# Kernel tuning notes

Measured on AMD Instinct MI355X. Metric: run time of the kernel, lower is better.

## Reference

```python
import jax, jax.numpy as jnp
import numpy as np

IN_FEATURES = 4096
OUT_FEATURES = 16384
BATCH, SEQ = 4, 2048


def setup_inputs() -> dict:
    key = jax.random.key(0)
    k_x, k_w, k_b = jax.random.split(key, 3)
    x = jax.random.normal(k_x, (BATCH, SEQ, IN_FEATURES), dtype=jnp.float32)
    # int8-valued quantized weight stored as int32 for portability (values in [-128, 127])
    weight_quantized = jax.random.randint(k_w, (OUT_FEATURES, IN_FEATURES), -128, 128, dtype=jnp.int32)
    weight_scale = jnp.float32(0.01)        # scalar scale (symmetric quant)
    weight_zero_point = jnp.float32(0.0)    # scalar zero point
    bias = jax.random.normal(k_b, (OUT_FEATURES,), dtype=jnp.float32)
    return {
        "x": x,
        "weight_quantized": weight_quantized,
        "weight_scale": weight_scale,
        "weight_zero_point": weight_zero_point,
        "bias": bias,
    }


def reference(x, weight_quantized, weight_scale, weight_zero_point, bias):
    # dequantize: (q - zero_point) * scale  -> fp32 weight [out, in]
    weight = (weight_quantized.astype(jnp.float32) - weight_zero_point) * weight_scale
    # F.linear: y = x @ W^T + b ; x: [b, s, in], W: [out, in] -> y: [b, s, out]
    return jnp.einsum("bsi,oi->bso", x, weight) + bias
```

## Files before the change

### kernel.cpp

```cpp
#include <hip/hip_runtime.h>
#include <hip/hip_bf16.h>
#include <cstdint>


#define M_DIM 8192
#define N_DIM 16384
#define K_DIM 4096
#define BK    128
#define NT    (K_DIM / BK)

using i32x4 = __attribute__((ext_vector_type(4))) int;

__global__ __launch_bounds__(256) void quant_x_kernel(const float* __restrict__ x,
                                                      signed char* __restrict__ xq,
                                                      float* __restrict__ rs1,
                                                      float* __restrict__ rs2) {
    const int row = blockIdx.x;
    const float* xr = x + (size_t)row * K_DIM;
    const int tid = threadIdx.x;

    float4 v[4];
    float amax = 0.f;
    #pragma unroll
    for (int j = 0; j < 4; ++j) {
        v[j] = *(const float4*)(xr + j * 1024 + tid * 4);
        amax = fmaxf(amax, fmaxf(fmaxf(fabsf(v[j].x), fabsf(v[j].y)),
                                 fmaxf(fabsf(v[j].z), fabsf(v[j].w))));
    }
    #pragma unroll
    for (int off = 32; off > 0; off >>= 1)
        amax = fmaxf(amax, __shfl_xor(amax, off));
    __shared__ float smax[4];
    __shared__ int   ssum[4];
    const int wv = tid >> 6, ln = tid & 63;
    if (ln == 0) smax[wv] = amax;
    __syncthreads();
    amax = fmaxf(fmaxf(smax[0], smax[1]), fmaxf(smax[2], smax[3]));
    const float s   = amax * (1.0f / 127.0f);
    const float inv = amax > 0.f ? 127.0f / amax : 0.f;

    int sum = 0;
    #pragma unroll
    for (int j = 0; j < 4; ++j) {
        int q0 = (int)__builtin_rintf(v[j].x * inv);
        int q1 = (int)__builtin_rintf(v[j].y * inv);
        int q2 = (int)__builtin_rintf(v[j].z * inv);
        int q3 = (int)__builtin_rintf(v[j].w * inv);
        sum += q0 + q1 + q2 + q3;
        int packed = (q0 & 255) | ((q1 & 255) << 8) | ((q2 & 255) << 16) | ((q3 & 255) << 24);
        *(int*)(xq + (size_t)row * K_DIM + j * 1024 + tid * 4) = packed;
    }
    #pragma unroll
    for (int off = 32; off > 0; off >>= 1)
        sum += __shfl_xor(sum, off);
    if (ln == 0) ssum[wv] = sum;
    __syncthreads();
    if (tid == 0) {
        int t = ssum[0] + ssum[1] + ssum[2] + ssum[3];
        rs1[row] = s;
        rs2[row] = s * (float)t;
    }
}

__global__ void quant_w_kernel(const int* __restrict__ q, signed char* __restrict__ o,
                               long long n) {
    long long i = ((long long)blockIdx.x * blockDim.x + threadIdx.x) * 4;
    const long long stride = (long long)gridDim.x * blockDim.x * 4;
    for (; i < n; i += stride) {
        int4 v = *(const int4*)(q + i);
        int packed = (v.x & 255) | ((v.y & 255) << 8) | ((v.z & 255) << 16) | ((v.w & 255) << 24);
        *(int*)(o + i) = packed;
    }
}

#define SB() __builtin_amdgcn_sched_barrier(0)

__device__ __forceinline__ void barrier_() {
    SB();
    asm volatile("" ::: "memory");
    __builtin_amdgcn_s_barrier();
    asm volatile("" ::: "memory");
    SB();
}

__device__ __forceinline__ void stage_half(const signed char* g0, unsigned char* l0) {
    __builtin_amdgcn_global_load_lds((const __attribute__((address_space(1))) void*)g0,
                                     (__attribute__((address_space(3))) void*)l0, 16, 0, 0);
    __builtin_amdgcn_global_load_lds(
        (const __attribute__((address_space(1))) void*)(g0 + (size_t)64 * K_DIM),
        (__attribute__((address_space(3))) void*)(l0 + 8192), 16, 0, 0);
}

__global__ __launch_bounds__(512, 2) void gemm_i8_kernel(const signed char* __restrict__ A,
                                                         const signed char* __restrict__ B,
                                                         const float* __restrict__ rs1,
                                                         const float* __restrict__ rs2,
                                                         const float* __restrict__ scale,
                                                         const float* __restrict__ zpp,
                                                         const float* __restrict__ bias,
                                                         float* __restrict__ C) {
    extern __shared__ unsigned char smem[];

    const int tid  = threadIdx.x;
    const int wave = tid >> 6;
    const int lane = tid & 63;
    const int fr = lane & 15, kq = lane >> 4;
    const int wr = wave >> 2, wc = wave & 3;

    const int swz = (blockIdx.x & 7) * 256 + (blockIdx.x >> 3);
    const int ntn = N_DIM / 256;
    const int tileRow = (swz / ntn) * 256;
    const int tileCol = (swz % ntn) * 256;

    const size_t goff = (size_t)(tid >> 3) * K_DIM + (((tid & 7) ^ ((tid >> 3) & 7)) * 16);
    const signed char* Au  = A + (size_t)tileRow * K_DIM + goff;
    const signed char* Bu  = B + (size_t)tileCol * K_DIM + goff;
    const signed char* AuH = Au + (size_t)128 * K_DIM;
    const signed char* BuH = Bu + (size_t)128 * K_DIM;

    const int aoffB = wr * 16384 + fr * 128;
    const int boffB = 32768 + wc * 8192 + fr * 128;
    int cs[2];
    #pragma unroll
    for (int kh = 0; kh < 2; ++kh)
        cs[kh] = ((kh * 4 + kq) ^ (fr & 7)) * 16;

    i32x4 acc[8][4] = {};
    i32x4 arA[4], arB[4], b0[2], b1[2];

    {
        unsigned char* w0 = smem + wave * 1024;
        unsigned char* w1 = smem + 65536 + wave * 1024;
        stage_half(Au,  w0);
        stage_half(AuH, w0 + 16384);
        stage_half(Bu,  w0 + 32768);
        stage_half(BuH, w0 + 49152);
        stage_half(Bu + BK,  w1 + 32768);
        stage_half(BuH + BK, w1 + 49152);
        stage_half(Au + BK,  w1);
        stage_half(AuH + BK, w1 + 16384);
    }
    SB();
    asm volatile("s_waitcnt vmcnt(8)" ::: "memory");
    barrier_();

    for (int t = 0; t < NT; ++t) {
        const unsigned char* cb = smem + (t & 1) * 65536;
        unsigned char* sw = smem + (t & 1) * 65536 + wave * 1024;
        const int kn2 = (t + 2) * BK;
        const bool st = (t + 2 < NT);

        #pragma unroll
        for (int kh = 0; kh < 2; ++kh) {
            const int c = cs[kh];

            #pragma unroll
            for (int m = 0; m < 4; ++m)
                arA[m] = *(const i32x4*)(cb + aoffB + m * 2048 + c);
            #pragma unroll
            for (int n = 0; n < 2; ++n)
                b0[n] = *(const i32x4*)(cb + boffB + n * 2048 + c);
            barrier_();
            asm volatile("s_waitcnt lgkmcnt(0)" ::: "memory");
            SB();
            __builtin_amdgcn_s_setprio(1);
            #pragma unroll
            for (int m = 0; m < 4; ++m)
                #pragma unroll
                for (int n = 0; n < 2; ++n)
                    acc[m][n] = __builtin_amdgcn_mfma_i32_16x16x64_i8(arA[m], b0[n], acc[m][n], 0, 0, 0);
            __builtin_amdgcn_s_setprio(0);
            barrier_();

            #pragma unroll
            for (int n = 0; n < 2; ++n)
                b1[n] = *(const i32x4*)(cb + boffB + (n + 2) * 2048 + c);
            barrier_();
            asm volatile("s_waitcnt lgkmcnt(0)" ::: "memory");
            SB();
            __builtin_amdgcn_s_setprio(1);
            #pragma unroll
            for (int m = 0; m < 4; ++m)
                #pragma unroll
                for (int n = 0; n < 2; ++n)
                    acc[m][n + 2] = __builtin_amdgcn_mfma_i32_16x16x64_i8(arA[m], b1[n], acc[m][n + 2], 0, 0, 0);
            __builtin_amdgcn_s_setprio(0);
            barrier_();

            #pragma unroll
            for (int m = 0; m < 4; ++m)
                arB[m] = *(const i32x4*)(cb + aoffB + (m + 4) * 2048 + c);
            if (kh == 1 && st) {
                stage_half(Bu + kn2,  sw + 32768);
                stage_half(BuH + kn2, sw + 49152);
            }
            barrier_();
            asm volatile("s_waitcnt lgkmcnt(0)" ::: "memory");
            SB();
            __builtin_amdgcn_s_setprio(1);
            #pragma unroll
            for (int m = 0; m < 4; ++m)
                #pragma unroll
                for (int n = 0; n < 2; ++n)
                    acc[m + 4][n + 2] = __builtin_amdgcn_mfma_i32_16x16x64_i8(arB[m], b1[n], acc[m + 4][n + 2], 0, 0, 0);
            __builtin_amdgcn_s_setprio(0);
            barrier_();

            if (kh == 1 && st) {
                stage_half(Au + kn2,  sw);
                stage_half(AuH + kn2, sw + 16384);
            }
            barrier_();
            __builtin_amdgcn_s_setprio(1);
            #pragma unroll
            for (int m = 0; m < 4; ++m)
                #pragma unroll
                for (int n = 0; n < 2; ++n)
                    acc[m + 4][n] = __builtin_amdgcn_mfma_i32_16x16x64_i8(arB[m], b0[n], acc[m + 4][n], 0, 0, 0);
            __builtin_amdgcn_s_setprio(0);
            SB();
            if (kh == 1) {
                if (st) {
                    asm volatile("s_waitcnt vmcnt(8)" ::: "memory");
                } else if (t + 1 < NT) {
                    asm volatile("s_waitcnt vmcnt(0)" ::: "memory");
                }
            }
            barrier_();
        }
    }

    const float swv = scale[0];
    const float zpv = zpp[0];
    float bv[4];
    #pragma unroll
    for (int n = 0; n < 4; ++n)
        bv[n] = bias[tileCol + wc * 64 + n * 16 + fr];
    #pragma unroll
    for (int m = 0; m < 8; ++m) {
        #pragma unroll
        for (int j = 0; j < 4; ++j) {
            const int grow = tileRow + wr * 128 + m * 16 + kq * 4 + j;
            const float f1 = rs1[grow] * swv;
            const float f2 = zpv * rs2[grow] * swv;
            float* Crow = C + (size_t)grow * N_DIM + tileCol + wc * 64 + fr;
            #pragma unroll
            for (int n = 0; n < 4; ++n)
                Crow[n * 16] = f1 * (float)acc[m][n][j] - f2 + bv[n];
        }
    }
}

__global__ void gemm_naive(const float* __restrict__ x, const int* __restrict__ wq,
                           const float* __restrict__ sp, const float* __restrict__ zp,
                           const float* __restrict__ bias, float* __restrict__ out) {
    __shared__ float sX[32][33];
    __shared__ float sW[32][33];
    const float s = sp[0], z = zp[0];
    const int tx = threadIdx.x & 15, ty = threadIdx.x >> 4;
    const int row0 = blockIdx.y * 32, col0 = blockIdx.x * 32;
    float acc[2][2] = {};
    for (int k0 = 0; k0 < K_DIM; k0 += 32) {
        for (int i = threadIdx.x; i < 32 * 32; i += 256) {
            int r = i >> 5, cc2 = i & 31;
            sX[r][cc2] = x[(size_t)(row0 + r) * K_DIM + k0 + cc2];
            sW[r][cc2] = ((float)wq[(size_t)(col0 + r) * K_DIM + k0 + cc2] - z) * s;
        }
        __syncthreads();
        #pragma unroll
        for (int k = 0; k < 32; ++k) {
            float xa0 = sX[ty * 2][k], xa1 = sX[ty * 2 + 1][k];
            float wb0 = sW[tx * 2][k], wb1 = sW[tx * 2 + 1][k];
            acc[0][0] += xa0 * wb0; acc[0][1] += xa0 * wb1;
            acc[1][0] += xa1 * wb0; acc[1][1] += xa1 * wb1;
        }
        __syncthreads();
    }
    #pragma unroll
    for (int i = 0; i < 2; ++i)
        #pragma unroll
        for (int j = 0; j < 2; ++j)
            out[(size_t)(row0 + ty * 2 + i) * N_DIM + (col0 + tx * 2 + j)] =
                acc[i][j] + bias[col0 + tx * 2 + j];
}

extern "C" void kernel_launch(void* const* d_in, const int* in_sizes, int n_in,
                              void* d_out, int out_size, void* d_ws, size_t ws_size,
                              hipStream_t stream) {
    const float* x     = (const float*)d_in[0];
    const int*   wq    = (const int*)d_in[1];
    const float* scale = (const float*)d_in[2];
    const float* zp    = (const float*)d_in[3];
    const float* bias  = (const float*)d_in[4];
    float* out = (float*)d_out;

    const size_t offXq = 0;
    const size_t offWq = (size_t)M_DIM * K_DIM;
    const size_t offR1 = offWq + (size_t)N_DIM * K_DIM;
    const size_t offR2 = offR1 + (size_t)M_DIM * sizeof(float);
    const size_t need  = offR2 + (size_t)M_DIM * sizeof(float);

    if (ws_size >= need) {
        signed char* xq  = (signed char*)d_ws + offXq;
        signed char* wq8 = (signed char*)d_ws + offWq;
        float* rs1 = (float*)((char*)d_ws + offR1);
        float* rs2 = (float*)((char*)d_ws + offR2);
        quant_x_kernel<<<M_DIM, 256, 0, stream>>>(x, xq, rs1, rs2);
        quant_w_kernel<<<4096, 256, 0, stream>>>(wq, wq8, (long long)N_DIM * K_DIM);
        (void)hipFuncSetAttribute((const void*)gemm_i8_kernel,
                                  hipFuncAttributeMaxDynamicSharedMemorySize, 131072);
        gemm_i8_kernel<<<(M_DIM / 256) * (N_DIM / 256), 512, 131072, stream>>>(
            xq, wq8, rs1, rs2, scale, zp, bias, out);
    } else {
        dim3 grid(N_DIM / 32, M_DIM / 32);
        gemm_naive<<<grid, 256, 0, stream>>>(x, wq, scale, zp, bias, out);
    }
}
```

Measured before the change: 681.8 us.

## Merge quantization kernels and simplify GEMM main loop to one-ahead prefetch

Merges the activation-quantization and weight-packing kernels into one launch that splits work by block index, saving one launch and letting both phases run concurrently. The GEMM main loop drops its two-stage-ahead interleaved schedule, which split MFMAs into four barrier-separated quadrants with staged loads between them. It now issues the next tile's global-to-LDS loads at the top of each iteration, loads all A/B fragments at once, runs the full 8x4 MFMA block, and waits for the loads with one barrier per tile. This cuts barrier count but shortens the prefetch distance and raises register pressure, so latency hiding may suffer.

```diff
diff --git a/kernel.cpp b/kernel.cpp
--- a/kernel.cpp
+++ b/kernel.cpp
@@ -11,65 +11,65 @@
 
 using i32x4 = __attribute__((ext_vector_type(4))) int;
 
-__global__ __launch_bounds__(256) void quant_x_kernel(const float* __restrict__ x,
-                                                      signed char* __restrict__ xq,
-                                                      float* __restrict__ rs1,
-                                                      float* __restrict__ rs2) {
-    const int row = blockIdx.x;
-    const float* xr = x + (size_t)row * K_DIM;
+__global__ __launch_bounds__(256) void prep_kernel(const float* __restrict__ x,
+                                                   const int* __restrict__ q,
+                                                   signed char* __restrict__ xq,
+                                                   signed char* __restrict__ wq8,
+                                                   float* __restrict__ rs1,
+                                                   float* __restrict__ rs2) {
     const int tid = threadIdx.x;
-
-    float4 v[4];
-    float amax = 0.f;
-    #pragma unroll
-    for (int j = 0; j < 4; ++j) {
-        v[j] = *(const float4*)(xr + j * 1024 + tid * 4);
-        amax = fmaxf(amax, fmaxf(fmaxf(fabsf(v[j].x), fabsf(v[j].y)),
-                                 fmaxf(fabsf(v[j].z), fabsf(v[j].w))));
-    }
-    #pragma unroll
-    for (int off = 32; off > 0; off >>= 1)
-        amax = fmaxf(amax, __shfl_xor(amax, off));
-    __shared__ float smax[4];
-    __shared__ int   ssum[4];
-    const int wv = tid >> 6, ln = tid & 63;
-    if (ln == 0) smax[wv] = amax;
-    __syncthreads();
-    amax = fmaxf(fmaxf(smax[0], smax[1]), fmaxf(smax[2], smax[3]));
-    const float s   = amax * (1.0f / 127.0f);
-    const float inv = amax > 0.f ? 127.0f / amax : 0.f;
-
-    int sum = 0;
-    #pragma unroll
-    for (int j = 0; j < 4; ++j) {
-        int q0 = (int)__builtin_rintf(v[j].x * inv);
-        int q1 = (int)__builtin_rintf(v[j].y * inv);
-        int q2 = (int)__builtin_rintf(v[j].z * inv);
-        int q3 = (int)__builtin_rintf(v[j].w * inv);
-        sum += q0 + q1 + q2 + q3;
-        int packed = (q0 & 255) | ((q1 & 255) << 8) | ((q2 & 255) << 16) | ((q3 & 255) << 24);
-        *(int*)(xq + (size_t)row * K_DIM + j * 1024 + tid * 4) = packed;
-    }
-    #pragma unroll
-    for (int off = 32; off > 0; off >>= 1)
-        sum += __shfl_xor(sum, off);
-    if (ln == 0) ssum[wv] = sum;
-    __syncthreads();
-    if (tid == 0) {
-        int t = ssum[0] + ssum[1] + ssum[2] + ssum[3];
-        rs1[row] = s;
-        rs2[row] = s * (float)t;
-    }
-}
-
-__global__ void quant_w_kernel(const int* __restrict__ q, signed char* __restrict__ o,
-                               long long n) {
-    long long i = ((long long)blockIdx.x * blockDim.x + threadIdx.x) * 4;
-    const long long stride = (long long)gridDim.x * blockDim.x * 4;
-    for (; i < n; i += stride) {
-        int4 v = *(const int4*)(q + i);
-        int packed = (v.x & 255) | ((v.y & 255) << 8) | ((v.z & 255) << 16) | ((v.w & 255) << 24);
-        *(int*)(o + i) = packed;
+    if (blockIdx.x < M_DIM) {
+        const int row = blockIdx.x;
+        const float* xr = x + (size_t)row * K_DIM;
+        float4 v[4];
+        float amax = 0.f;
+        #pragma unroll
+        for (int j = 0; j < 4; ++j) {
+            v[j] = *(const float4*)(xr + j * 1024 + tid * 4);
+            amax = fmaxf(amax, fmaxf(fmaxf(fabsf(v[j].x), fabsf(v[j].y)),
+                                     fmaxf(fabsf(v[j].z), fabsf(v[j].w))));
+        }
+        #pragma unroll
+        for (int off = 32; off > 0; off >>= 1)
+            amax = fmaxf(amax, __shfl_xor(amax, off));
+        __shared__ float smax[4];
+        __shared__ int   ssum[4];
+        const int wv = tid >> 6, ln = tid & 63;
+        if (ln == 0) smax[wv] = amax;
+        __syncthreads();
+        amax = fmaxf(fmaxf(smax[0], smax[1]), fmaxf(smax[2], smax[3]));
+        const float s   = amax * (1.0f / 127.0f);
+        const float inv = amax > 0.f ? 127.0f / amax : 0.f;
+        int sum = 0;
+        #pragma unroll
+        for (int j = 0; j < 4; ++j) {
+            int q0 = (int)__builtin_rintf(v[j].x * inv);
+            int q1 = (int)__builtin_rintf(v[j].y * inv);
+            int q2 = (int)__builtin_rintf(v[j].z * inv);
+            int q3 = (int)__builtin_rintf(v[j].w * inv);
+            sum += q0 + q1 + q2 + q3;
+            int packed = (q0 & 255) | ((q1 & 255) << 8) | ((q2 & 255) << 16) | ((q3 & 255) << 24);
+            *(int*)(xq + (size_t)row * K_DIM + j * 1024 + tid * 4) = packed;
+        }
+        #pragma unroll
+        for (int off = 32; off > 0; off >>= 1)
+            sum += __shfl_xor(sum, off);
+        if (ln == 0) ssum[wv] = sum;
+        __syncthreads();
+        if (tid == 0) {
+            int t = ssum[0] + ssum[1] + ssum[2] + ssum[3];
+            rs1[row] = s;
+            rs2[row] = s * (float)t;
+        }
+    } else {
+        const long long n = (long long)N_DIM * K_DIM;
+        long long i = (((long long)(blockIdx.x - M_DIM)) * 256 + tid) * 4;
+        const long long stride = (long long)4096 * 256 * 4;
+        for (; i < n; i += stride) {
+            int4 v = *(const int4*)(q + i);
+            int packed = (v.x & 255) | ((v.y & 255) << 8) | ((v.z & 255) << 16) | ((v.w & 255) << 24);
+            *(int*)(wq8 + i) = packed;
+        }
     }
 }
 
@@ -126,108 +126,54 @@
         cs[kh] = ((kh * 4 + kq) ^ (fr & 7)) * 16;
 
     i32x4 acc[8][4] = {};
-    i32x4 arA[4], arB[4], b0[2], b1[2];
 
     {
         unsigned char* w0 = smem + wave * 1024;
-        unsigned char* w1 = smem + 65536 + wave * 1024;
         stage_half(Au,  w0);
         stage_half(AuH, w0 + 16384);
         stage_half(Bu,  w0 + 32768);
         stage_half(BuH, w0 + 49152);
-        stage_half(Bu + BK,  w1 + 32768);
-        stage_half(BuH + BK, w1 + 49152);
-        stage_half(Au + BK,  w1);
-        stage_half(AuH + BK, w1 + 16384);
     }
     SB();
-    asm volatile("s_waitcnt vmcnt(8)" ::: "memory");
+    asm volatile("s_waitcnt vmcnt(0)" ::: "memory");
     barrier_();
 
     for (int t = 0; t < NT; ++t) {
         const unsigned char* cb = smem + (t & 1) * 65536;
-        unsigned char* sw = smem + (t & 1) * 65536 + wave * 1024;
-        const int kn2 = (t + 2) * BK;
-        const bool st = (t + 2 < NT);
+        unsigned char* ow = smem + ((t + 1) & 1) * 65536 + wave * 1024;
+        const int kn1 = (t + 1) * BK;
+
+        if (t + 1 < NT) {
+            stage_half(Au + kn1,  ow);
+            stage_half(AuH + kn1, ow + 16384);
+            stage_half(Bu + kn1,  ow + 32768);
+            stage_half(BuH + kn1, ow + 49152);
+        }
 
         #pragma unroll
         for (int kh = 0; kh < 2; ++kh) {
             const int c = cs[kh];
-
-            #pragma unroll
-            for (int m = 0; m < 4; ++m)
-                arA[m] = *(const i32x4*)(cb + aoffB + m * 2048 + c);
-            #pragma unroll
-            for (int n = 0; n < 2; ++n)
-                b0[n] = *(const i32x4*)(cb + boffB + n * 2048 + c);
-            barrier_();
+            i32x4 a[8], b[4];
+            #pragma unroll
+            for (int m = 0; m < 8; ++m)
+                a[m] = *(const i32x4*)(cb + aoffB + m * 2048 + c);
+            #pragma unroll
+            for (int n = 0; n < 4; ++n)
+                b[n] = *(const i32x4*)(cb + boffB + n * 2048 + c);
             asm volatile("s_waitcnt lgkmcnt(0)" ::: "memory");
             SB();
             __builtin_amdgcn_s_setprio(1);
             #pragma unroll
-            for (int m = 0; m < 4; ++m)
+            for (int m = 0; m < 8; ++m)
                 #pragma unroll
-                for (int n = 0; n < 2; ++n)
-                    acc[m][n] = __builtin_amdgcn_mfma_i32_16x16x64_i8(arA[m], b0[n], acc[m][n], 0, 0, 0);
+                for (int n = 0; n < 4; ++n)
+                    acc[m][n] = __builtin_amdgcn_mfma_i32_16x16x64_i8(a[m], b[n], acc[m][n], 0, 0, 0);
             __builtin_amdgcn_s_setprio(0);
-            barrier_();
-
-            #pragma unroll
-            for (int n = 0; n < 2; ++n)
-                b1[n] = *(const i32x4*)(cb + boffB + (n + 2) * 2048 + c);
-            barrier_();
-            asm volatile("s_waitcnt lgkmcnt(0)" ::: "memory");
-            SB();
-            __builtin_amdgcn_s_setprio(1);
-            #pragma unroll
-            for (int m = 0; m < 4; ++m)
-                #pragma unroll
-                for (int n = 0; n < 2; ++n)
-                    acc[m][n + 2] = __builtin_amdgcn_mfma_i32_16x16x64_i8(arA[m], b1[n], acc[m][n + 2], 0, 0, 0);
-            __builtin_amdgcn_s_setprio(0);
-            barrier_();
-
-            #pragma unroll
-            for (int m = 0; m < 4; ++m)
-                arB[m] = *(const i32x4*)(cb + aoffB + (m + 4) * 2048 + c);
-            if (kh == 1 && st) {
-                stage_half(Bu + kn2,  sw + 32768);
-                stage_half(BuH + kn2, sw + 49152);
-            }
-            barrier_();
-            asm volatile("s_waitcnt lgkmcnt(0)" ::: "memory");
-            SB();
-            __builtin_amdgcn_s_setprio(1);
-            #pragma unroll
-            for (int m = 0; m < 4; ++m)
-                #pragma unroll
-                for (int n = 0; n < 2; ++n)
-                    acc[m + 4][n + 2] = __builtin_amdgcn_mfma_i32_16x16x64_i8(arB[m], b1[n], acc[m + 4][n + 2], 0, 0, 0);
-            __builtin_amdgcn_s_setprio(0);
-            barrier_();
-
-            if (kh == 1 && st) {
-                stage_half(Au + kn2,  sw);
-                stage_half(AuH + kn2, sw + 16384);
-            }
-            barrier_();
-            __builtin_amdgcn_s_setprio(1);
-            #pragma unroll
-            for (int m = 0; m < 4; ++m)
-                #pragma unroll
-                for (int n = 0; n < 2; ++n)
-                    acc[m + 4][n] = __builtin_amdgcn_mfma_i32_16x16x64_i8(arB[m], b0[n], acc[m + 4][n], 0, 0, 0);
-            __builtin_amdgcn_s_setprio(0);
-            SB();
-            if (kh == 1) {
-                if (st) {
-                    asm volatile("s_waitcnt vmcnt(8)" ::: "memory");
-                } else if (t + 1 < NT) {
-                    asm volatile("s_waitcnt vmcnt(0)" ::: "memory");
-                }
-            }
-            barrier_();
-        }
+        }
+
+        SB();
+        asm volatile("s_waitcnt vmcnt(0)" ::: "memory");
+        barrier_();
     }
 
     const float swv = scale[0];
@@ -305,8 +251,7 @@
         signed char* wq8 = (signed char*)d_ws + offWq;
         float* rs1 = (float*)((char*)d_ws + offR1);
         float* rs2 = (float*)((char*)d_ws + offR2);
-        quant_x_kernel<<<M_DIM, 256, 0, stream>>>(x, xq, rs1, rs2);
-        quant_w_kernel<<<4096, 256, 0, stream>>>(wq, wq8, (long long)N_DIM * K_DIM);
+        prep_kernel<<<M_DIM + 4096, 256, 0, stream>>>(x, wq, xq, wq8, rs1, rs2);
         (void)hipFuncSetAttribute((const void*)gemm_i8_kernel,
                                   hipFuncAttributeMaxDynamicSharedMemorySize, 131072);
         gemm_i8_kernel<<<(M_DIM / 256) * (N_DIM / 256), 512, 131072, stream>>>(
```

Result: faster. 659.0 us (-3.3%).
